# Performance work log

Hardware: AMD Instinct MI355X
Metric: run time of the kernel (lower is better)

Reference implementation:

```python
import jax, jax.numpy as jnp
import numpy as np

V, E, H, K = 50000, 256, 512, 32
START, STOP = 30, 31
B, T = 32, 256
NEG = -10000.0


def _lstm_dir(x, W_ih, W_hh, b, h0, c0):
    # x: [T,B,E] -> outputs [T,B,H]; PyTorch gate order i,f,g,o
    xw = jnp.einsum('tbe,ge->tbg', x, W_ih) + b  # [T,B,4H]
    def step(carry, xw_t):
        h, c = carry
        z = xw_t + h @ W_hh.T
        i, f, g, o = jnp.split(z, 4, axis=-1)
        c = jax.nn.sigmoid(f) * c + jax.nn.sigmoid(i) * jnp.tanh(g)
        h = jax.nn.sigmoid(o) * jnp.tanh(c)
        return (h, c), h
    (_, _), hs = jax.lax.scan(step, (h0, c0), xw)
    return hs


def setup_inputs() -> dict:
    key = jax.random.key(0)
    ks = jax.random.split(key, 13)
    sc = 0.05
    sentence = jax.random.randint(ks[0], (B, T), 0, V)
    emb = jax.random.normal(ks[1], (V, E), jnp.float32) * 0.1
    W_ih_f = jax.random.normal(ks[2], (4 * H, E), jnp.float32) * sc
    W_hh_f = jax.random.normal(ks[3], (4 * H, H), jnp.float32) * sc
    b_f = jax.random.normal(ks[4], (4 * H,), jnp.float32) * sc
    W_ih_b = jax.random.normal(ks[5], (4 * H, E), jnp.float32) * sc
    W_hh_b = jax.random.normal(ks[6], (4 * H, H), jnp.float32) * sc
    b_b = jax.random.normal(ks[7], (4 * H,), jnp.float32) * sc
    W_out = jax.random.normal(ks[8], (K, 2 * H), jnp.float32) * sc
    b_out = jax.random.normal(ks[9], (K,), jnp.float32) * sc
    transitions = jax.random.normal(ks[10], (K, K), jnp.float32)
    transitions = transitions.at[START, :].set(NEG).at[:, STOP].set(NEG)
    h0 = jax.random.normal(ks[11], (2, B, H), jnp.float32)
    c0 = jax.random.normal(ks[12], (2, B, H), jnp.float32)
    return dict(sentence=sentence, emb=emb, W_ih_f=W_ih_f, W_hh_f=W_hh_f, b_f=b_f,
                W_ih_b=W_ih_b, W_hh_b=W_hh_b, b_b=b_b, W_out=W_out, b_out=b_out,
                transitions=transitions, h0=h0, c0=c0)


def reference(sentence, emb, W_ih_f, W_hh_f, b_f, W_ih_b, W_hh_b, b_b,
              W_out, b_out, transitions, h0, c0):
    batch, seqlen = sentence.shape
    ntag = transitions.shape[0]
    # embedding (dropout = identity at inference), time-major
    x = emb[sentence].transpose(1, 0, 2)  # [T,B,E]
    hf = _lstm_dir(x, W_ih_f, W_hh_f, b_f, h0[0], c0[0])
    hb = _lstm_dir(x[::-1], W_ih_b, W_hh_b, b_b, h0[1], c0[1])[::-1]
    rnn_out = jnp.concatenate([hf, hb], axis=-1).transpose(1, 0, 2)  # [B,T,2H]
    feats = rnn_out @ W_out.T + b_out  # [B,T,K]

    # Viterbi decode, vectorized over batch and tags
    v0 = jnp.full((batch, ntag), NEG, feats.dtype).at[:, START].set(0.0)
    def vstep(v, feat_t):
        # scores[b, next, prev] = v[b, prev] + transitions[next, prev]
        scores = v[:, None, :] + transitions[None, :, :]
        bp = jnp.argmax(scores, axis=-1)              # [B,K] best prev per next
        v_new = jnp.max(scores, axis=-1) + feat_t     # [B,K]
        return v_new, bp
    v, bps = jax.lax.scan(vstep, v0, feats.transpose(1, 0, 2))  # bps: [T,B,K]

    terminal = v + transitions[STOP]                  # [B,K]
    best_last = jnp.argmax(terminal, axis=-1)         # [B]
    path_score = jnp.take_along_axis(terminal, best_last[:, None], axis=1)[:, 0]

    def back(tag, bp_t):
        prev = jnp.take_along_axis(bp_t, tag[:, None], axis=1)[:, 0]
        return prev, tag
    _, path = jax.lax.scan(back, best_last, bps, reverse=True)  # [T,B], time order
    best_path = path.transpose(1, 0)                  # [B,T]
    return path_score, best_path
```

## Files before the change

kernel.cpp:

```cpp
#include <hip/hip_runtime.h>
#include <hip/hip_bf16.h>
#include <cstdint>


typedef __attribute__((ext_vector_type(8)))  short          s8v;
typedef __attribute__((ext_vector_type(8)))  __bf16         bf8v;
typedef __attribute__((ext_vector_type(16))) float          f32x16;
typedef __attribute__((ext_vector_type(4)))  float          f32x4v;
typedef __attribute__((ext_vector_type(4)))  unsigned int   u32x4;
typedef __attribute__((ext_vector_type(8)))  unsigned short u16x8;
typedef __attribute__((ext_vector_type(4)))  unsigned short u16x4;

template <typename V>
static __device__ inline auto mfma_try(V a, V b, f32x16 c, int)
    -> decltype(__builtin_amdgcn_mfma_f32_32x32x16_bf16(a, b, c, 0, 0, 0)) {
  return __builtin_amdgcn_mfma_f32_32x32x16_bf16(a, b, c, 0, 0, 0);
}
template <typename V>
static __device__ inline f32x16 mfma_try(V a, V b, f32x16 c, long) {
  return __builtin_amdgcn_mfma_f32_32x32x16_bf16(
      __builtin_bit_cast(bf8v, a), __builtin_bit_cast(bf8v, b), c, 0, 0, 0);
}
static __device__ inline f32x16 mfma32(u16x8 a, u16x8 b, f32x16 c) {
  return mfma_try(__builtin_bit_cast(s8v, a), __builtin_bit_cast(s8v, b), c, 0);
}

static __device__ inline unsigned short bf_trunc(float x) {
  return (unsigned short)(__builtin_bit_cast(unsigned int, x) >> 16);
}
static __device__ inline float bf_up(unsigned short h) {
  return __builtin_bit_cast(float, ((unsigned int)h) << 16);
}
static __device__ inline void split2(float x, unsigned short& hi, unsigned short& lo) {
  hi = bf_trunc(x);
  lo = bf_trunc(x - bf_up(hi));
}
static __device__ inline float sigmoidf_(float x) { return 1.0f / (1.0f + __expf(-x)); }
static __device__ inline float tanhf_(float x) {
  float ax = fabsf(x);
  float e  = __expf(-2.0f * ax);
  float t  = (1.0f - e) / (1.0f + e);
  return x < 0.0f ? -t : t;
}

static __device__ inline u32x4 ld16(const void* p) {
  u32x4 r;
  asm volatile("global_load_dwordx4 %0, %1, off" : "=v"(r) : "v"(p) : "memory");
  return r;
}
static __device__ inline u32x4 ld_cohere16(const void* p) {
  u32x4 r;
  asm volatile("global_load_dwordx4 %0, %1, off sc0 sc1" : "=v"(r) : "v"(p) : "memory");
  return r;
}
static __device__ inline void st_cohere2(void* p, unsigned short v) {
  asm volatile("global_store_short %0, %1, off sc0 sc1" :: "v"(p), "v"(v) : "memory");
}
static __device__ inline void st_cohere4(void* p, int v) {
  asm volatile("global_store_dword %0, %1, off sc0 sc1" :: "v"(p), "v"(v) : "memory");
}
#define WAITVM(N)                                              \
  do {                                                         \
    asm volatile("s_waitcnt vmcnt(" #N ")" ::: "memory");      \
    __builtin_amdgcn_sched_barrier(0);                         \
  } while (0)

__global__ void k_embed(const int* __restrict__ sent, const float* __restrict__ emb,
                        unsigned short* __restrict__ xhi, unsigned short* __restrict__ xlo) {
  int row  = blockIdx.x * 4 + (threadIdx.x >> 6);
  int lane = threadIdx.x & 63;
  int t = row >> 5, b = row & 31;
  int tok = sent[b * 256 + t];
  const f32x4v v = *(const f32x4v*)(emb + (long)tok * 256 + lane * 4);
  u16x4 h4, l4;
#pragma unroll
  for (int i = 0; i < 4; ++i) {
    unsigned short h, l;
    split2(v[i], h, l);
    h4[i] = h; l4[i] = l;
  }
  *(u16x4*)(xhi + (long)row * 256 + lane * 4) = h4;
  *(u16x4*)(xlo + (long)row * 256 + lane * 4) = l4;
}

__global__ __launch_bounds__(256, 1) void k_lstm(
    const float* __restrict__ Whh_f, const float* __restrict__ Whh_b,
    const float* __restrict__ Wih_f, const float* __restrict__ Wih_b,
    const float* __restrict__ b_f,   const float* __restrict__ b_b,
    const float* __restrict__ h0,    const float* __restrict__ c0,
    const unsigned short* __restrict__ xhi, const unsigned short* __restrict__ xlo,
    unsigned short* __restrict__ hbhi, unsigned short* __restrict__ hblo,
    unsigned short* __restrict__ hshi, unsigned short* __restrict__ hslo,
    int* __restrict__ flags) {
  const int tid = threadIdx.x, lane = tid & 63, w = tid >> 6;
  const int blk = blockIdx.x, dir = blk >> 6, b64 = blk & 63;
  const float* Whh  = dir ? Whh_b : Whh_f;
  const float* Wih  = dir ? Wih_b : Wih_f;
  const float* bias = dir ? b_b   : b_f;

  __shared__ float zp[4][32][33];

  const int n  = lane & 31;
  const int kh = lane >> 5;
  const int wrow = ((n >> 3) << 9) + (b64 << 3) + (n & 7);

  u16x8 wbh[8], wbl[8];
#pragma unroll
  for (int k8 = 0; k8 < 8; ++k8) {
    const float* src = Whh + (long)wrow * 512 + (w << 7) + (k8 << 4) + (kh << 3);
    f32x4v a = *(const f32x4v*)src, b2 = *(const f32x4v*)(src + 4);
    u16x8 hh, ll;
#pragma unroll
    for (int i = 0; i < 8; ++i) {
      float v = (i < 4) ? a[i] : b2[i - 4];
      unsigned short x1, x2; split2(v, x1, x2);
      hh[i] = x1; ll[i] = x2;
    }
    wbh[k8] = hh; wbl[k8] = ll;
  }
  u16x8 wih_h[4], wih_l[4];
#pragma unroll
  for (int k4 = 0; k4 < 4; ++k4) {
    const float* src = Wih + (long)wrow * 256 + (w << 6) + (k4 << 4) + (kh << 3);
    f32x4v a = *(const f32x4v*)src, b2 = *(const f32x4v*)(src + 4);
    u16x8 hh, ll;
#pragma unroll
    for (int i = 0; i < 8; ++i) {
      float v = (i < 4) ? a[i] : b2[i - 4];
      unsigned short x1, x2; split2(v, x1, x2);
      hh[i] = x1; ll[i] = x2;
    }
    wih_h[k4] = hh; wih_l[k4] = ll;
  }

  const int gb = tid & 31;
  const int gi = tid >> 5;
  const int gidx = (b64 << 3) + gi;
  float c = c0[(dir * 32 + gb) * 512 + gidx];
  float bias4[4];
#pragma unroll
  for (int g = 0; g < 4; ++g) bias4[g] = bias[(g << 9) + gidx];

  {
    float hv = h0[(dir * 32 + gb) * 512 + gidx];
    unsigned short hh, ll; split2(hv, hh, ll);
    int off = ((0 * 2 + dir) * 64 + b64) * 256 + gb * 8 + gi;
    st_cohere2(hbhi + off, hh);
    st_cohere2(hblo + off, ll);
  }
  WAITVM(0);
  __syncthreads();
  if (tid == 0) st_cohere4(flags + dir * 64 + b64, 1);

  const int m = lane & 31;

  for (int step = 0; step < 256; ++step) {
    const int t = dir ? (255 - step) : step;

    u32x4 xah_[4], xal_[4];
#pragma unroll
    for (int k4 = 0; k4 < 4; ++k4) {
      long ro = (long)(t * 32 + m) * 256 + (w << 6) + (k4 << 4) + (kh << 3);
      xah_[k4] = ld16(xhi + ro);
      xal_[k4] = ld16(xlo + ro);
    }

    {
      const int* fl = flags + dir * 64;
      const int tgt = step + 1;
      while (true) {
        int fv = __hip_atomic_load(fl + lane, __ATOMIC_RELAXED, __HIP_MEMORY_SCOPE_AGENT);
        if (__all(fv >= tgt)) break;
      }
    }

    const int pr = step & 1;
    const unsigned short* hb_hi = hbhi + ((pr * 2 + dir) * 64) * 256;
    const unsigned short* hb_lo = hblo + ((pr * 2 + dir) * 64) * 256;
    u32x4 ah_[8], al_[8];
#pragma unroll
    for (int k8 = 0; k8 < 8; ++k8) {
      int bs = (w << 4) + (k8 << 1) + kh;
      ah_[k8] = ld_cohere16(hb_hi + bs * 256 + m * 8);
      al_[k8] = ld_cohere16(hb_lo + bs * 256 + m * 8);
    }

    WAITVM(16);
    f32x16 acc0 = (f32x16)0.0f, acc1 = (f32x16)0.0f;
#pragma unroll
    for (int k4 = 0; k4 < 4; ++k4) {
      u16x8 xa = __builtin_bit_cast(u16x8, xah_[k4]);
      u16x8 xl = __builtin_bit_cast(u16x8, xal_[k4]);
      if (k4 & 1) {
        acc1 = mfma32(xa, wih_h[k4], acc1);
        acc0 = mfma32(xa, wih_l[k4], acc0);
        acc1 = mfma32(xl, wih_h[k4], acc1);
      } else {
        acc0 = mfma32(xa, wih_h[k4], acc0);
        acc1 = mfma32(xa, wih_l[k4], acc1);
        acc0 = mfma32(xl, wih_h[k4], acc0);
      }
    }

    WAITVM(8);
#pragma unroll
    for (int k8 = 0; k8 < 4; ++k8) {
      u16x8 ah = __builtin_bit_cast(u16x8, ah_[k8]);
      u16x8 al = __builtin_bit_cast(u16x8, al_[k8]);
      if (k8 & 1) {
        acc1 = mfma32(ah, wbh[k8], acc1);
        acc0 = mfma32(ah, wbl[k8], acc0);
        acc1 = mfma32(al, wbh[k8], acc1);
      } else {
        acc0 = mfma32(ah, wbh[k8], acc0);
        acc1 = mfma32(ah, wbl[k8], acc1);
        acc0 = mfma32(al, wbh[k8], acc0);
      }
    }
    WAITVM(0);
#pragma unroll
    for (int k8 = 4; k8 < 8; ++k8) {
      u16x8 ah = __builtin_bit_cast(u16x8, ah_[k8]);
      u16x8 al = __builtin_bit_cast(u16x8, al_[k8]);
      if (k8 & 1) {
        acc1 = mfma32(ah, wbh[k8], acc1);
        acc0 = mfma32(ah, wbl[k8], acc0);
        acc1 = mfma32(al, wbh[k8], acc1);
      } else {
        acc0 = mfma32(ah, wbh[k8], acc0);
        acc1 = mfma32(ah, wbl[k8], acc1);
        acc0 = mfma32(al, wbh[k8], acc0);
      }
    }

#pragma unroll
    for (int r = 0; r < 16; ++r) {
      int mr = (r & 3) + ((r >> 2) << 3) + (kh << 2);
      zp[w][mr][n] = acc0[r] + acc1[r];
    }
    __syncthreads();

    float z[4];
#pragma unroll
    for (int g = 0; g < 4; ++g)
      z[g] = zp[0][gb][g * 8 + gi] + zp[1][gb][g * 8 + gi] +
             zp[2][gb][g * 8 + gi] + zp[3][gb][g * 8 + gi] + bias4[g];
    float ig = sigmoidf_(z[0]);
    float fg = sigmoidf_(z[1]);
    float gg = tanhf_(z[2]);
    float og = sigmoidf_(z[3]);
    c = fg * c + ig * gg;
    float nh = og * tanhf_(c);

    unsigned short hh, ll; split2(nh, hh, ll);
    const int pw = (step + 1) & 1;
    int off = ((pw * 2 + dir) * 64 + b64) * 256 + gb * 8 + gi;
    st_cohere2(hbhi + off, hh);
    st_cohere2(hblo + off, ll);
    long ho = ((long)(dir * 256 + t) * 64 + b64) * 256 + gb * 8 + gi;
    hshi[ho] = hh; hslo[ho] = ll;

    WAITVM(0);
    __syncthreads();
    if (tid == 0) st_cohere4(flags + dir * 64 + b64, step + 2);
  }
}

__global__ __launch_bounds__(256, 1) void k_feats(
    const unsigned short* __restrict__ hshi, const unsigned short* __restrict__ hslo,
    const float* __restrict__ Wout, const float* __restrict__ bout,
    float* __restrict__ feats) {
  const int tid = threadIdx.x, lane = tid & 63, w = tid >> 6;
  const int t = blockIdx.x;
  __shared__ float zp[4][32][33];
  const int n = lane & 31, kh = lane >> 5;
  const int dirw = w >> 1, koff = (w & 1) * 256;

  u16x8 bh[16], bl[16];
#pragma unroll
  for (int k = 0; k < 16; ++k) {
    const float* src = Wout + (long)n * 1024 + dirw * 512 + koff + (k << 4) + (kh << 3);
    f32x4v a = *(const f32x4v*)src, b2 = *(const f32x4v*)(src + 4);
    u16x8 hh, ll;
#pragma unroll
    for (int i = 0; i < 8; ++i) {
      float v = (i < 4) ? a[i] : b2[i - 4];
      unsigned short x1, x2; split2(v, x1, x2);
      hh[i] = x1; ll[i] = x2;
    }
    bh[k] = hh; bl[k] = ll;
  }

  const int m = lane & 31;
  f32x16 acc = (f32x16)0.0f;
  const unsigned short* base_h = hshi + ((long)(dirw * 256 + t) * 64) * 256;
  const unsigned short* base_l = hslo + ((long)(dirw * 256 + t) * 64) * 256;
#pragma unroll
  for (int k = 0; k < 16; ++k) {
    int ksrc = koff + (k << 4) + (kh << 3);
    int bs = ksrc >> 3;
    u16x8 ah = *(const u16x8*)(base_h + bs * 256 + m * 8);
    u16x8 al = *(const u16x8*)(base_l + bs * 256 + m * 8);
    acc = mfma32(ah, bh[k], acc);
    acc = mfma32(ah, bl[k], acc);
    acc = mfma32(al, bh[k], acc);
  }
#pragma unroll
  for (int r = 0; r < 16; ++r) {
    int mr = (r & 3) + ((r >> 2) << 3) + (kh << 2);
    zp[w][mr][n] = acc[r];
  }
  __syncthreads();

  const int k = tid & 31, mb = tid >> 5;
#pragma unroll
  for (int q = 0; q < 4; ++q) {
    int mm = mb * 4 + q;
    float v = zp[0][mm][k] + zp[1][mm][k] + zp[2][mm][k] + zp[3][mm][k] + bout[k];
    feats[((long)mm * 256 + t) * 32 + k] = v;
  }
}

__global__ __launch_bounds__(64, 1) void k_viterbi(const float* __restrict__ feats,
                                                   const float* __restrict__ trans,
                                                   float* __restrict__ out) {
  const int b = blockIdx.x, lane = threadIdx.x;
  __shared__ __align__(16) float fsh[256][32];
  __shared__ unsigned char bp[256][32];

  const float* fb = feats + (long)b * 8192;
#pragma unroll 4
  for (int i = lane; i < 2048; i += 64)
    ((f32x4v*)&fsh[0][0])[i] = ((const f32x4v*)fb)[i];

  float tr_[32];
  float vl = 0.0f;
  if (lane < 32) {
#pragma unroll
    for (int p = 0; p < 32; ++p) tr_[p] = trans[lane * 32 + p];
    vl = (lane == 30) ? 0.0f : -10000.0f;
  }
  __syncthreads();

  if (lane < 32) {
    for (int t = 0; t < 256; ++t) {
      float best = -3.0e38f; int arg = 0;
#pragma unroll
      for (int p = 0; p < 32; ++p) {
        float vp = __shfl(vl, p, 32);
        float sc = vp + tr_[p];
        if (sc > best) { best = sc; arg = p; }
      }
      vl = best + fsh[t][lane];
      bp[t][lane] = (unsigned char)arg;
    }
    float tv = vl + trans[31 * 32 + lane];
    int ta = lane;
#pragma unroll
    for (int d = 16; d; d >>= 1) {
      float ov = __shfl_xor(tv, d, 32);
      int   oa = __shfl_xor(ta, d, 32);
      if (ov > tv || (ov == tv && oa < ta)) { tv = ov; ta = oa; }
    }
    if (lane == 0) {
      out[b] = tv;
      int tag = ta;
      for (int t = 255; t >= 0; --t) {
        out[32 + (long)b * 256 + t] = (float)tag;
        tag = bp[t][tag];
      }
    }
  }
}

extern "C" void kernel_launch(void* const* d_in, const int* in_sizes, int n_in,
                              void* d_out, int out_size, void* d_ws, size_t ws_size,
                              hipStream_t stream) {
  (void)in_sizes; (void)n_in; (void)out_size; (void)ws_size;
  const int*   sent  = (const int*)d_in[0];
  const float* emb   = (const float*)d_in[1];
  const float* Wih_f = (const float*)d_in[2];
  const float* Whh_f = (const float*)d_in[3];
  const float* b_f   = (const float*)d_in[4];
  const float* Wih_b = (const float*)d_in[5];
  const float* Whh_b = (const float*)d_in[6];
  const float* b_b   = (const float*)d_in[7];
  const float* Wout  = (const float*)d_in[8];
  const float* bout  = (const float*)d_in[9];
  const float* trans = (const float*)d_in[10];
  const float* h0    = (const float*)d_in[11];
  const float* c0    = (const float*)d_in[12];
  float* out = (float*)d_out;

  char* ws = (char*)d_ws;
  unsigned short* xhi  = (unsigned short*)(ws + 0);
  unsigned short* xlo  = (unsigned short*)(ws + (4ull << 20));
  unsigned short* hbhi = (unsigned short*)(ws + (8ull << 20));
  unsigned short* hblo = (unsigned short*)(ws + (8ull << 20) + (256ull << 10));
  unsigned short* hshi = (unsigned short*)(ws + (9ull << 20));
  unsigned short* hslo = (unsigned short*)(ws + (26ull << 20));
  float*          fts  = (float*)(ws + (43ull << 20));
  int*            flg  = (int*)(ws + (45ull << 20));

  hipMemsetAsync(flg, 0, 128 * sizeof(int), stream);
  k_embed<<<2048, 256, 0, stream>>>(sent, emb, xhi, xlo);
  k_lstm<<<128, 256, 0, stream>>>(Whh_f, Whh_b, Wih_f, Wih_b, b_f, b_b, h0, c0,
                                  xhi, xlo, hbhi, hblo, hshi, hslo, flg);
  k_feats<<<256, 256, 0, stream>>>(hshi, hslo, Wout, bout, fts);
  k_viterbi<<<32, 64, 0, stream>>>(fts, trans, out);
}
```

Baseline: 1.260 ms.

## Stage hidden state in LDS, store one wide vector, prefetch next-step inputs

```diff
diff --git a/kernel.cpp b/kernel.cpp
--- a/kernel.cpp
+++ b/kernel.cpp
@@ -53,8 +53,8 @@
   asm volatile("global_load_dwordx4 %0, %1, off sc0 sc1" : "=v"(r) : "v"(p) : "memory");
   return r;
 }
-static __device__ inline void st_cohere2(void* p, unsigned short v) {
-  asm volatile("global_store_short %0, %1, off sc0 sc1" :: "v"(p), "v"(v) : "memory");
+static __device__ inline void st_cohere16(void* p, u32x4 v) {
+  asm volatile("global_store_dwordx4 %0, %1, off sc0 sc1" :: "v"(p), "v"(v) : "memory");
 }
 static __device__ inline void st_cohere4(void* p, int v) {
   asm volatile("global_store_dword %0, %1, off sc0 sc1" :: "v"(p), "v"(v) : "memory");
@@ -89,9 +89,7 @@
     const float* __restrict__ b_f,   const float* __restrict__ b_b,
     const float* __restrict__ h0,    const float* __restrict__ c0,
     const unsigned short* __restrict__ xhi, const unsigned short* __restrict__ xlo,
-    unsigned short* __restrict__ hbhi, unsigned short* __restrict__ hblo,
-    unsigned short* __restrict__ hshi, unsigned short* __restrict__ hslo,
-    int* __restrict__ flags) {
+    unsigned short* __restrict__ hist, int* __restrict__ flags) {
   const int tid = threadIdx.x, lane = tid & 63, w = tid >> 6;
   const int blk = blockIdx.x, dir = blk >> 6, b64 = blk & 63;
   const float* Whh  = dir ? Whh_b : Whh_f;
@@ -99,6 +97,7 @@
   const float* bias = dir ? b_b   : b_f;
 
   __shared__ float zp[4][32][33];
+  __shared__ __align__(16) unsigned short hstage[512];
 
   const int n  = lane & 31;
   const int kh = lane >> 5;
@@ -144,48 +143,35 @@
   {
     float hv = h0[(dir * 32 + gb) * 512 + gidx];
     unsigned short hh, ll; split2(hv, hh, ll);
-    int off = ((0 * 2 + dir) * 64 + b64) * 256 + gb * 8 + gi;
-    st_cohere2(hbhi + off, hh);
-    st_cohere2(hblo + off, ll);
-  }
-  WAITVM(0);
+    hstage[gb * 8 + gi] = hh;
+    hstage[256 + gb * 8 + gi] = ll;
+  }
+  __syncthreads();
+  if (w == 0) {
+    const u32x4* hs = (const u32x4*)hstage;
+    u32x4 v = hs[lane];
+    char* dst = (char*)hist + (((long)dir * 257 + 0) * 64 + b64) * 1024 + lane * 16;
+    st_cohere16(dst, v);
+    WAITVM(0);
+  }
   __syncthreads();
   if (tid == 0) st_cohere4(flags + dir * 64 + b64, 1);
 
   const int m = lane & 31;
 
-  for (int step = 0; step < 256; ++step) {
-    const int t = dir ? (255 - step) : step;
-
-    u32x4 xah_[4], xal_[4];
+  u32x4 xah_[4], xal_[4];
+  {
+    const int t0 = dir ? 255 : 0;
 #pragma unroll
     for (int k4 = 0; k4 < 4; ++k4) {
-      long ro = (long)(t * 32 + m) * 256 + (w << 6) + (k4 << 4) + (kh << 3);
+      long ro = (long)(t0 * 32 + m) * 256 + (w << 6) + (k4 << 4) + (kh << 3);
       xah_[k4] = ld16(xhi + ro);
       xal_[k4] = ld16(xlo + ro);
     }
-
-    {
-      const int* fl = flags + dir * 64;
-      const int tgt = step + 1;
-      while (true) {
-        int fv = __hip_atomic_load(fl + lane, __ATOMIC_RELAXED, __HIP_MEMORY_SCOPE_AGENT);
-        if (__all(fv >= tgt)) break;
-      }
-    }
-
-    const int pr = step & 1;
-    const unsigned short* hb_hi = hbhi + ((pr * 2 + dir) * 64) * 256;
-    const unsigned short* hb_lo = hblo + ((pr * 2 + dir) * 64) * 256;
-    u32x4 ah_[8], al_[8];
-#pragma unroll
-    for (int k8 = 0; k8 < 8; ++k8) {
-      int bs = (w << 4) + (k8 << 1) + kh;
-      ah_[k8] = ld_cohere16(hb_hi + bs * 256 + m * 8);
-      al_[k8] = ld_cohere16(hb_lo + bs * 256 + m * 8);
-    }
-
-    WAITVM(16);
+  }
+
+  for (int step = 0; step < 256; ++step) {
+    WAITVM(0);
     f32x16 acc0 = (f32x16)0.0f, acc1 = (f32x16)0.0f;
 #pragma unroll
     for (int k4 = 0; k4 < 4; ++k4) {
@@ -201,6 +187,25 @@
         acc0 = mfma32(xl, wih_h[k4], acc0);
       }
     }
+    __builtin_amdgcn_sched_barrier(0);
+
+    {
+      const int* fl = flags + dir * 64;
+      const int tgt = step + 1;
+      while (true) {
+        int fv = __hip_atomic_load(fl + lane, __ATOMIC_RELAXED, __HIP_MEMORY_SCOPE_AGENT);
+        if (__all(fv >= tgt)) break;
+      }
+    }
+
+    const unsigned short* hb = hist + (((long)dir * 257 + step) * 64) * 512;
+    u32x4 ah_[8], al_[8];
+#pragma unroll
+    for (int k8 = 0; k8 < 8; ++k8) {
+      int bs = (w << 4) + (k8 << 1) + kh;
+      ah_[k8] = ld_cohere16(hb + bs * 512 + m * 8);
+      al_[k8] = ld_cohere16(hb + bs * 512 + 256 + m * 8);
+    }
 
     WAITVM(8);
 #pragma unroll
@@ -251,23 +256,35 @@
     float og = sigmoidf_(z[3]);
     c = fg * c + ig * gg;
     float nh = og * tanhf_(c);
-
     unsigned short hh, ll; split2(nh, hh, ll);
-    const int pw = (step + 1) & 1;
-    int off = ((pw * 2 + dir) * 64 + b64) * 256 + gb * 8 + gi;
-    st_cohere2(hbhi + off, hh);
-    st_cohere2(hblo + off, ll);
-    long ho = ((long)(dir * 256 + t) * 64 + b64) * 256 + gb * 8 + gi;
-    hshi[ho] = hh; hslo[ho] = ll;
-
-    WAITVM(0);
+
+    if (step < 255) {
+      const int tn = dir ? (254 - step) : (step + 1);
+#pragma unroll
+      for (int k4 = 0; k4 < 4; ++k4) {
+        long ro = (long)(tn * 32 + m) * 256 + (w << 6) + (k4 << 4) + (kh << 3);
+        xah_[k4] = ld16(xhi + ro);
+        xal_[k4] = ld16(xlo + ro);
+      }
+    }
+
+    hstage[gb * 8 + gi] = hh;
+    hstage[256 + gb * 8 + gi] = ll;
+    __syncthreads();
+    if (w == 0) {
+      const u32x4* hs = (const u32x4*)hstage;
+      u32x4 v = hs[lane];
+      char* dst = (char*)hist + (((long)dir * 257 + step + 1) * 64 + b64) * 1024 + lane * 16;
+      st_cohere16(dst, v);
+      WAITVM(0);
+    }
     __syncthreads();
     if (tid == 0) st_cohere4(flags + dir * 64 + b64, step + 2);
   }
 }
 
 __global__ __launch_bounds__(256, 1) void k_feats(
-    const unsigned short* __restrict__ hshi, const unsigned short* __restrict__ hslo,
+    const unsigned short* __restrict__ hist,
     const float* __restrict__ Wout, const float* __restrict__ bout,
     float* __restrict__ feats) {
   const int tid = threadIdx.x, lane = tid & 63, w = tid >> 6;
@@ -292,15 +309,15 @@
   }
 
   const int m = lane & 31;
+  const int slot = dirw ? (256 - t) : (t + 1);
+  const unsigned short* base = hist + (((long)dirw * 257 + slot) * 64) * 512;
   f32x16 acc = (f32x16)0.0f;
-  const unsigned short* base_h = hshi + ((long)(dirw * 256 + t) * 64) * 256;
-  const unsigned short* base_l = hslo + ((long)(dirw * 256 + t) * 64) * 256;
 #pragma unroll
   for (int k = 0; k < 16; ++k) {
     int ksrc = koff + (k << 4) + (kh << 3);
     int bs = ksrc >> 3;
-    u16x8 ah = *(const u16x8*)(base_h + bs * 256 + m * 8);
-    u16x8 al = *(const u16x8*)(base_l + bs * 256 + m * 8);
+    u16x8 ah = *(const u16x8*)(base + bs * 512 + m * 8);
+    u16x8 al = *(const u16x8*)(base + bs * 512 + 256 + m * 8);
     acc = mfma32(ah, bh[k], acc);
     acc = mfma32(ah, bl[k], acc);
     acc = mfma32(al, bh[k], acc);
@@ -395,17 +412,14 @@
   char* ws = (char*)d_ws;
   unsigned short* xhi  = (unsigned short*)(ws + 0);
   unsigned short* xlo  = (unsigned short*)(ws + (4ull << 20));
-  unsigned short* hbhi = (unsigned short*)(ws + (8ull << 20));
-  unsigned short* hblo = (unsigned short*)(ws + (8ull << 20) + (256ull << 10));
-  unsigned short* hshi = (unsigned short*)(ws + (9ull << 20));
-  unsigned short* hslo = (unsigned short*)(ws + (26ull << 20));
-  float*          fts  = (float*)(ws + (43ull << 20));
-  int*            flg  = (int*)(ws + (45ull << 20));
+  unsigned short* hist = (unsigned short*)(ws + (8ull << 20));
+  float*          fts  = (float*)(ws + (42ull << 20));
+  int*            flg  = (int*)(ws + (44ull << 20));
 
   hipMemsetAsync(flg, 0, 128 * sizeof(int), stream);
   k_embed<<<2048, 256, 0, stream>>>(sent, emb, xhi, xlo);
   k_lstm<<<128, 256, 0, stream>>>(Whh_f, Whh_b, Wih_f, Wih_b, b_f, b_b, h0, c0,
-                                  xhi, xlo, hbhi, hblo, hshi, hslo, flg);
-  k_feats<<<256, 256, 0, stream>>>(hshi, hslo, Wout, bout, fts);
+                                  xhi, xlo, hist, flg);
+  k_feats<<<256, 256, 0, stream>>>(hist, Wout, bout, fts);
   k_viterbi<<<32, 64, 0, stream>>>(fts, trans, out);
 }
```

New measurement: 1.542 ms. 1.22x slower.
